# Performance work log

Measured on AMD Instinct MI355X. Metric: run time of the kernel, lower is better.

Reference implementation:

```python
import jax, jax.numpy as jnp
import numpy as np

N = 50000      # nodes
E = 800000     # edges
D = 256        # num_feat == num_hidden == out_dim
G = 64         # graphs in batch
C = 64         # num_classes
L = 2          # cells (layers)
S = 2          # GNN steps per cell
SCALE = 0.05


def setup_inputs() -> dict:
    key = jax.random.key(0)
    ks = jax.random.split(key, 10)
    x = jax.random.normal(ks[0], (N, D), jnp.float32)
    edge_index = jax.random.randint(ks[1], (2, E), 0, N, dtype=jnp.int64)
    edge_attr = jax.random.normal(ks[2], (E, 1), jnp.float32)
    batch = jnp.sort(jax.random.randint(ks[3], (N,), 0, G, dtype=jnp.int64))
    pre_w = jax.random.normal(ks[4], (L, 2, D, D), jnp.float32) * SCALE
    pre_b = jax.random.normal(ks[5], (L, 2, D), jnp.float32) * SCALE
    gcn_w = jax.random.normal(ks[6], (L, S, D, D), jnp.float32) * SCALE
    gcn_b = jax.random.normal(ks[7], (L, S, D), jnp.float32) * SCALE
    cls_w = jax.random.normal(ks[8], (D, C), jnp.float32) * SCALE
    cls_b = jax.random.normal(ks[9], (C,), jnp.float32) * SCALE
    return {"x": x, "edge_index": edge_index, "edge_attr": edge_attr,
            "batch": batch, "pre_w": pre_w, "pre_b": pre_b,
            "gcn_w": gcn_w, "gcn_b": gcn_b, "cls_w": cls_w, "cls_b": cls_b}


def reference(x, edge_index, edge_attr, batch, pre_w, pre_b, gcn_w, gcn_b, cls_w, cls_b):
    n = x.shape[0]
    # GCNConv with self-loops and symmetric normalization (torch_geometric default)
    loops = jnp.arange(n, dtype=edge_index.dtype)
    src = jnp.concatenate([edge_index[0], loops])   # [E+N]
    dst = jnp.concatenate([edge_index[1], loops])   # [E+N]
    deg = jax.ops.segment_sum(jnp.ones_like(dst, dtype=x.dtype), dst, num_segments=n)
    dinv = jax.lax.rsqrt(deg)                        # deg >= 1 due to self loops
    norm = (dinv[src] * dinv[dst])[:, None]          # [E+N, 1]

    def gcn(h, w, b):
        hw = h @ w                                   # [N, D]
        msg = hw[src] * norm                         # gather + scale
        return jax.ops.segment_sum(msg, dst, num_segments=n) + b

    def cell(s0, s1, l):
        s0 = s0 @ pre_w[l, 0] + pre_b[l, 0]
        s1 = s1 @ pre_w[l, 1] + pre_b[l, 1]
        states = [s0, s1]
        for i, idx in enumerate((0, 1)):             # NAS indices [0, 1]
            states.append(gcn(states[idx], gcn_w[l, i], gcn_b[l, i]))
        # concat='add': tmp = states[2]; then accumulate states[2:] again
        tmp = states[2]
        for st in states[2:]:
            tmp = tmp + st                           # = 2*s2 + s3 (faithful)
        return tmp

    s0 = s1 = x
    for l in range(L):
        s0, s1 = s1, cell(s0, s1, l)
    out = s1                                         # [N, D]

    g = cls_b.shape[0] if False else G
    counts = jax.ops.segment_sum(jnp.ones((n,), x.dtype), batch, num_segments=G)
    mean_pool = jax.ops.segment_sum(out, batch, num_segments=G) / jnp.maximum(counts, 1.0)[:, None]
    max_pool = jax.ops.segment_max(out, batch, num_segments=G)
    max_pool = jnp.where(counts[:, None] > 0, max_pool, 0.0)
    pooled = mean_pool + max_pool                    # [G, D]
    return pooled @ cls_w + cls_b                    # [G, C]
```

## Files before the change

### kernel.cpp

```cpp
#include <hip/hip_runtime.h>

typedef __attribute__((ext_vector_type(8))) short bf16x8;
typedef __attribute__((ext_vector_type(4))) float f32x4;

__device__ inline float bf2f(unsigned short u) {
    union { float f; unsigned int i; } v; v.i = ((unsigned int)u) << 16; return v.f;
}
__device__ inline unsigned short f2bf(float f) {
    union { float f; unsigned int u; } v; v.f = f;
    unsigned int x = v.u;
    unsigned int r = x + 0x7FFFu + ((x >> 16) & 1u);
    return (unsigned short)(r >> 16);
}
__device__ inline unsigned int fenc(float x) {
    union { float f; unsigned int u; } v; v.f = x;
    return (v.u & 0x80000000u) ? ~v.u : (v.u | 0x80000000u);
}
__device__ inline float fdec(unsigned int k) {
    union { float f; unsigned int u; } v;
    v.u = (k & 0x80000000u) ? (k & 0x7FFFFFFFu) : ~k;
    return v.f;
}
__device__ inline float ldf(const void* p, size_t i, int f32) {
    return f32 ? ((const float*)p)[i] : bf2f(((const unsigned short*)p)[i]);
}
__device__ inline int ldi(const int* p, size_t i, int i64) {
    return i64 ? p[2 * i] : p[i];
}

__global__ __launch_bounds__(256)
void k_detect(const unsigned short* __restrict__ xu, int xstride,
              const int* __restrict__ ei, int estride, int* __restrict__ flags) {
    __shared__ int cnt, orv;
    if (threadIdx.x == 0) { cnt = 0; orv = 0; }
    __syncthreads();
    int c = 0, o = 0;
    for (int s = 0; s < 4; ++s) {
        int j = threadIdx.x * 4 + s;
        size_t k = (size_t)j * xstride;
        unsigned short u = xu[2 * k];
        int e = (u >> 7) & 0xFF;
        if (e >= 100 && e <= 140) ++c;
        size_t idx = (size_t)j * estride;
        o |= ei[2 * idx + 1];
    }
    atomicAdd(&cnt, c); atomicOr(&orv, o);
    __syncthreads();
    if (threadIdx.x == 0) {
        flags[0] = (cnt < 768) ? 1 : 0;
        flags[1] = (orv == 0) ? 1 : 0;
    }
}

__global__ void k_zero(int* __restrict__ hist, int* __restrict__ cursor,
                       float* __restrict__ psum, unsigned int* __restrict__ pkey,
                       int* __restrict__ pcnt, int N) {
    int t = blockIdx.x * 256 + threadIdx.x;
    if (t < N) hist[t] = 0;
    else if (t < 2 * N) cursor[t - N] = 0;
    else if (t < 2 * N + 16384) psum[t - 2 * N] = 0.f;
    else if (t < 2 * N + 32768) pkey[t - 2 * N - 16384] = 0u;
    else if (t < 2 * N + 32768 + 64) pcnt[t - 2 * N - 32768] = 0;
}

__global__ __launch_bounds__(256)
void k_cvt(const void* __restrict__ X, unsigned short* __restrict__ Xb,
           size_t nelem, const int* __restrict__ flags) {
    int f = flags[0];
    size_t i = ((size_t)blockIdx.x * 256 + threadIdx.x) * 8;
    if (i >= nelem) return;
    if (f) {
        const float* s = (const float*)X + i;
        float4 f0 = *(const float4*)s;
        float4 f1 = *(const float4*)(s + 4);
        int4 o;
        o.x = (int)f2bf(f0.x) | ((int)f2bf(f0.y) << 16);
        o.y = (int)f2bf(f0.z) | ((int)f2bf(f0.w) << 16);
        o.z = (int)f2bf(f1.x) | ((int)f2bf(f1.y) << 16);
        o.w = (int)f2bf(f1.z) | ((int)f2bf(f1.w) << 16);
        *(int4*)(Xb + i) = o;
    } else {
        *(int4*)(Xb + i) = *(const int4*)((const unsigned short*)X + i);
    }
}

__global__ __launch_bounds__(256)
void k_cvtw(const void* __restrict__ pre_w, const void* __restrict__ gcn_w,
            unsigned short* __restrict__ Pb, unsigned short* __restrict__ Gt,
            const int* __restrict__ flags) {
    __shared__ float tile[64][65];
    const int i = blockIdx.y;
    const int m0 = (blockIdx.x & 3) * 64;
    const int n0 = (blockIdx.x >> 2) * 64;
    const int f = flags[0];
    const size_t base = (size_t)i * 65536;
#pragma unroll
    for (int q = 0; q < 16; ++q) {
        int idx = q * 256 + threadIdx.x;
        int r = idx >> 6, c = idx & 63;
        size_t src = base + (size_t)(m0 + r) * 256 + n0 + c;
        Pb[src] = f2bf(ldf(pre_w, src, f));
        tile[r][c] = ldf(gcn_w, src, f);
    }
    __syncthreads();
#pragma unroll
    for (int q = 0; q < 16; ++q) {
        int idx = q * 256 + threadIdx.x;
        int r = idx >> 6, c = idx & 63;
        Gt[base + (size_t)(n0 + r) * 256 + m0 + c] = f2bf(tile[c][r]);
    }
}

__global__ __launch_bounds__(256)
void k_prepw(const unsigned short* __restrict__ Pb, const unsigned short* __restrict__ Gt,
             unsigned short* __restrict__ Wt0, unsigned short* __restrict__ Wt1) {
    const int which = blockIdx.y;
    const int wid = threadIdx.x >> 6, lane = threadIdx.x & 63;
    const int tile = blockIdx.x * 4 + wid;
    const int n0 = (tile >> 4) * 16, k0 = (tile & 15) * 16;
    const int l15 = lane & 15, hi = lane >> 4;
    size_t base0, base1 = 0;
    if (which == 0)      { base0 = 0; base1 = 65536; }
    else if (which == 1) { base0 = 2 * 65536; }
    else                 { base0 = 3 * 65536; }
    f32x4 acc0 = {}, acc1 = {};
    const unsigned short* ga = Gt + base0 + (size_t)(n0 + l15) * 256 + hi * 8;
    const unsigned short* pa = Pb + base0 + (size_t)(k0 + l15) * 256 + hi * 8;
    const unsigned short* gb = Gt + base1 + (size_t)(n0 + l15) * 256 + hi * 8;
    const unsigned short* pb = Pb + base1 + (size_t)(k0 + l15) * 256 + hi * 8;
#pragma unroll
    for (int kt = 0; kt < 8; ++kt) {
        bf16x8 a0 = *(const bf16x8*)(ga + kt * 32);
        bf16x8 b0 = *(const bf16x8*)(pa + kt * 32);
        acc0 = __builtin_amdgcn_mfma_f32_16x16x32_bf16(a0, b0, acc0, 0, 0, 0);
        if (which == 0) {
            bf16x8 a1 = *(const bf16x8*)(gb + kt * 32);
            bf16x8 b1 = *(const bf16x8*)(pb + kt * 32);
            acc1 = __builtin_amdgcn_mfma_f32_16x16x32_bf16(a1, b1, acc1, 0, 0, 0);
        }
    }
#pragma unroll
    for (int j = 0; j < 4; ++j) {
        int n = n0 + hi * 4 + j;
        int k = k0 + l15;
        if (which == 0)      Wt0[(size_t)n * 256 + k]       = f2bf(2.f * acc0[j] + acc1[j]);
        else if (which == 1) Wt1[(size_t)n * 512 + k]       = f2bf(2.f * acc0[j]);
        else                 Wt1[(size_t)n * 512 + 256 + k] = f2bf(acc0[j]);
    }
}

__global__ __launch_bounds__(256)
void k_prepb(const void* __restrict__ pre_b, const unsigned short* __restrict__ Gt,
             const void* __restrict__ gcn_b,
             float* __restrict__ cvec, float* __restrict__ dvec,
             const int* __restrict__ flags) {
    __shared__ float pb[2][256];
    const int l = blockIdx.x, n = threadIdx.x;
    const int f = flags[0];
    pb[0][n] = ldf(pre_b, (size_t)(l * 2 + 0) * 256 + n, f);
    pb[1][n] = ldf(pre_b, (size_t)(l * 2 + 1) * 256 + n, f);
    __syncthreads();
    const unsigned short* g0 = Gt + (size_t)(l * 2 + 0) * 65536 + (size_t)n * 256;
    const unsigned short* g1 = Gt + (size_t)(l * 2 + 1) * 65536 + (size_t)n * 256;
    float a = 0.f, b = 0.f;
#pragma unroll 4
    for (int mc = 0; mc < 32; ++mc) {
        bf16x8 v0 = *(const bf16x8*)(g0 + mc * 8);
        bf16x8 v1 = *(const bf16x8*)(g1 + mc * 8);
#pragma unroll
        for (int u = 0; u < 8; ++u) {
            a += pb[0][mc * 8 + u] * bf2f((unsigned short)v0[u]);
            b += pb[1][mc * 8 + u] * bf2f((unsigned short)v1[u]);
        }
    }
    cvec[l * 256 + n] = 2.f * a + b;
    dvec[l * 256 + n] = 2.f * ldf(gcn_b, (size_t)(l * 2 + 0) * 256 + n, f)
                            + ldf(gcn_b, (size_t)(l * 2 + 1) * 256 + n, f);
}

__global__ void k_hist(const int* __restrict__ ei, int E, int N,
                       int* __restrict__ hist, const int* __restrict__ flags) {
    int e = blockIdx.x * 256 + threadIdx.x;
    if (e >= E) return;
    int i64 = flags[1];
    int d = ldi(ei, (size_t)E + e, i64); d = d < 0 ? 0 : (d >= N ? N - 1 : d);
    atomicAdd(&hist[d], 1);
}

__global__ __launch_bounds__(256)
void k_scan1(const int* __restrict__ hist, int* __restrict__ pre,
             int* __restrict__ bsum, int N) {
    __shared__ int s[256];
    int i = blockIdx.x * 256 + threadIdx.x;
    int v = (i < N) ? hist[i] : 0;
    s[threadIdx.x] = v;
    __syncthreads();
    for (int off = 1; off < 256; off <<= 1) {
        int t = (threadIdx.x >= off) ? s[threadIdx.x - off] : 0;
        __syncthreads();
        s[threadIdx.x] += t;
        __syncthreads();
    }
    if (i < N) pre[i] = s[threadIdx.x] - v;
    if (threadIdx.x == 255) bsum[blockIdx.x] = s[255];
}

__global__ __launch_bounds__(256)
void k_scan2(const int* __restrict__ bsum, int* __restrict__ boff,
             int* __restrict__ rowptr, int nb, int N) {
    __shared__ int s[256];
    int t = threadIdx.x;
    int v = (t < nb) ? bsum[t] : 0;
    s[t] = v;
    __syncthreads();
    for (int off = 1; off < 256; off <<= 1) {
        int x = (t >= off) ? s[t - off] : 0;
        __syncthreads();
        s[t] += x;
        __syncthreads();
    }
    if (t < nb) boff[t] = s[t] - v;
    if (t == nb - 1) rowptr[N] = s[t];
}

__global__ __launch_bounds__(256)
void k_scan3(const int* __restrict__ hist, const int* __restrict__ pre,
             const int* __restrict__ boff, int* __restrict__ rowptr,
             float* __restrict__ dinv, int N) {
    int i = blockIdx.x * 256 + threadIdx.x;
    if (i < N) {
        rowptr[i] = pre[i] + boff[blockIdx.x];
        dinv[i] = rsqrtf((float)(hist[i] + 1));
    }
}

__global__ void k_scatter(const int* __restrict__ ei, int E, int N,
                          const int* __restrict__ rowptr, int* __restrict__ cursor,
                          int* __restrict__ col, const int* __restrict__ flags) {
    int e = blockIdx.x * 256 + threadIdx.x;
    if (e >= E) return;
    int i64 = flags[1];
    int s = ldi(ei, (size_t)e, i64);     s = s < 0 ? 0 : (s >= N ? N - 1 : s);
    int d = ldi(ei, (size_t)E + e, i64); d = d < 0 ? 0 : (d >= N ? N - 1 : d);
    int pos = rowptr[d] + atomicAdd(&cursor[d], 1);
    col[pos] = s;
}

__global__ __launch_bounds__(512)
void k_gemm(const unsigned short* __restrict__ Xb, const unsigned short* __restrict__ Yb,
            const unsigned short* __restrict__ Wt, const float* __restrict__ cvec,
            const float* __restrict__ dinv, unsigned short* __restrict__ out,
            int M, int K) {
    __shared__ char ldsb[49152];
    const int tid = threadIdx.x;
    const int lane = tid & 63;
    const int wid = tid >> 6;
    const int wm = wid >> 2, wn = wid & 3;
    const int l15 = lane & 15, hi = lane >> 4;
    const int row0 = blockIdx.x * 128;

    const int ar = tid >> 3, acb = tid & 7;
    int agrow = row0 + ar; if (agrow > M - 1) agrow = M - 1;
    const size_t abase = (size_t)agrow * 256 + acb * 8;

    f32x4 acc[4][4] = {};
    const int KT = K / 64;
    int4 ra[2], rw[4];

    {
        const unsigned short* Asrc = Xb;
        ra[0] = *(const int4*)(Asrc + abase);
        {
            int id = 512 + tid; int r = id >> 3, cb = id & 7;
            int grow = row0 + r; if (grow > M - 1) grow = M - 1;
            ra[1] = *(const int4*)(Asrc + (size_t)grow * 256 + cb * 8);
        }
#pragma unroll
        for (int q = 0; q < 4; ++q) {
            int id = q * 512 + tid; int r = id >> 3, cb = id & 7;
            rw[q] = *(const int4*)(Wt + (size_t)r * K + cb * 8);
        }
    }

    for (int kt = 0; kt < KT; ++kt) {
        __syncthreads();
        {
            int sw = (acb * 16) ^ ((ar & 7) << 4);
            *(int4*)(ldsb + ar * 128 + sw) = ra[0];
            int id = 512 + tid; int r = id >> 3, cb = id & 7;
            int sw1 = (cb * 16) ^ ((r & 7) << 4);
            *(int4*)(ldsb + r * 128 + sw1) = ra[1];
        }
#pragma unroll
        for (int q = 0; q < 4; ++q) {
            int id = q * 512 + tid; int r = id >> 3, cb = id & 7;
            int sw = (cb * 16) ^ ((r & 7) << 4);
            *(int4*)(ldsb + 16384 + r * 128 + sw) = rw[q];
        }
        __syncthreads();
        if (kt + 1 < KT) {
            const int k1 = (kt + 1) * 64;
            const unsigned short* Asrc = (k1 < 256) ? Xb : Yb;
            const int ak1 = (k1 < 256) ? k1 : k1 - 256;
            ra[0] = *(const int4*)(Asrc + abase + ak1);
            {
                int id = 512 + tid; int r = id >> 3, cb = id & 7;
                int grow = row0 + r; if (grow > M - 1) grow = M - 1;
                ra[1] = *(const int4*)(Asrc + (size_t)grow * 256 + ak1 + cb * 8);
            }
#pragma unroll
            for (int q = 0; q < 4; ++q) {
                int id = q * 512 + tid; int r = id >> 3, cb = id & 7;
                rw[q] = *(const int4*)(Wt + (size_t)r * K + k1 + cb * 8);
            }
        }
#pragma unroll
        for (int kk = 0; kk < 2; ++kk) {
            bf16x8 af[4], bfr[4];
            int byte = kk * 64 + (hi << 4);
#pragma unroll
            for (int m = 0; m < 4; ++m) {
                int r = wm * 64 + m * 16 + l15;
                af[m] = *(const bf16x8*)(ldsb + r * 128 + (byte ^ ((r & 7) << 4)));
            }
#pragma unroll
            for (int n = 0; n < 4; ++n) {
                int r = wn * 64 + n * 16 + l15;
                bfr[n] = *(const bf16x8*)(ldsb + 16384 + r * 128 + (byte ^ ((r & 7) << 4)));
            }
#pragma unroll
            for (int m = 0; m < 4; ++m)
#pragma unroll
                for (int n = 0; n < 4; ++n)
                    acc[m][n] = __builtin_amdgcn_mfma_f32_16x16x32_bf16(af[m], bfr[n], acc[m][n], 0, 0, 0);
        }
    }
    for (int half = 0; half < 2; ++half) {
        __syncthreads();
        if (wm == half) {
#pragma unroll
            for (int m = 0; m < 4; ++m) {
#pragma unroll
                for (int j = 0; j < 4; ++j) {
                    int rl = m * 16 + hi * 4 + j;
                    int grow = row0 + half * 64 + rl;
                    if (grow < M) {
                        float di = dinv[grow];
#pragma unroll
                        for (int n = 0; n < 4; ++n) {
                            int colc = wn * 64 + n * 16 + l15;
                            float v = (acc[m][n][j] + cvec[colc]) * di;
                            *(unsigned short*)(ldsb + rl * 512 + colc * 2) = f2bf(v);
                        }
                    }
                }
            }
        }
        __syncthreads();
#pragma unroll
        for (int p = 0; p < 4; ++p) {
            int rl = p * 16 + (tid >> 5);
            int cb = tid & 31;
            int grow = row0 + half * 64 + rl;
            if (grow < M)
                *(int4*)(out + (size_t)grow * 256 + cb * 8) = *(const int4*)(ldsb + rl * 512 + cb * 16);
        }
    }
}

__global__ __launch_bounds__(256)
void k_agg(const unsigned short* __restrict__ U, const int* __restrict__ rowptr,
           const int* __restrict__ col, const float* __restrict__ dinv,
           const float* __restrict__ dvec, unsigned short* __restrict__ Y, int N) {
    int wave = (blockIdx.x * 256 + threadIdx.x) >> 6;
    int lane = threadIdx.x & 63;
    int nA = wave * 2, nB = nA + 1;
    if (nA >= N) return;
    const bool hasB = (nB < N);
    const size_t loff = (size_t)lane * 4;

    ushort4 sa = *(const ushort4*)(U + (size_t)nA * 256 + loff);
    float a0 = bf2f(sa.x), a1 = bf2f(sa.y), a2 = bf2f(sa.z), a3 = bf2f(sa.w);
    float b0 = 0.f, b1 = 0.f, b2 = 0.f, b3 = 0.f;
    int eA = rowptr[nA], endA = rowptr[nA + 1];
    int eB = 0, endB = 0;
    if (hasB) {
        ushort4 sb = *(const ushort4*)(U + (size_t)nB * 256 + loff);
        b0 = bf2f(sb.x); b1 = bf2f(sb.y); b2 = bf2f(sb.z); b3 = bf2f(sb.w);
        eB = rowptr[nB]; endB = rowptr[nB + 1];
    }

    while (eA + 8 <= endA && eB + 8 <= endB) {
        int sA[8], sB[8];
#pragma unroll
        for (int u = 0; u < 8; ++u) {
            sA[u] = __builtin_amdgcn_readfirstlane(col[eA + u]);
            sB[u] = __builtin_amdgcn_readfirstlane(col[eB + u]);
        }
        ushort4 vA[8], vB[8];
#pragma unroll
        for (int u = 0; u < 8; ++u) {
            vA[u] = *(const ushort4*)(U + (size_t)sA[u] * 256 + loff);
            vB[u] = *(const ushort4*)(U + (size_t)sB[u] * 256 + loff);
        }
#pragma unroll
        for (int u = 0; u < 8; ++u) {
            a0 += bf2f(vA[u].x); a1 += bf2f(vA[u].y);
            a2 += bf2f(vA[u].z); a3 += bf2f(vA[u].w);
            b0 += bf2f(vB[u].x); b1 += bf2f(vB[u].y);
            b2 += bf2f(vB[u].z); b3 += bf2f(vB[u].w);
        }
        eA += 8; eB += 8;
    }
    for (; eA + 8 <= endA; eA += 8) {
        int s[8]; ushort4 v[8];
#pragma unroll
        for (int u = 0; u < 8; ++u) s[u] = __builtin_amdgcn_readfirstlane(col[eA + u]);
#pragma unroll
        for (int u = 0; u < 8; ++u) v[u] = *(const ushort4*)(U + (size_t)s[u] * 256 + loff);
#pragma unroll
        for (int u = 0; u < 8; ++u) {
            a0 += bf2f(v[u].x); a1 += bf2f(v[u].y);
            a2 += bf2f(v[u].z); a3 += bf2f(v[u].w);
        }
    }
    for (; eA < endA; ++eA) {
        int s = __builtin_amdgcn_readfirstlane(col[eA]);
        ushort4 v = *(const ushort4*)(U + (size_t)s * 256 + loff);
        a0 += bf2f(v.x); a1 += bf2f(v.y); a2 += bf2f(v.z); a3 += bf2f(v.w);
    }
    if (hasB) {
        for (; eB + 8 <= endB; eB += 8) {
            int s[8]; ushort4 v[8];
#pragma unroll
            for (int u = 0; u < 8; ++u) s[u] = __builtin_amdgcn_readfirstlane(col[eB + u]);
#pragma unroll
            for (int u = 0; u < 8; ++u) v[u] = *(const ushort4*)(U + (size_t)s[u] * 256 + loff);
#pragma unroll
            for (int u = 0; u < 8; ++u) {
                b0 += bf2f(v[u].x); b1 += bf2f(v[u].y);
                b2 += bf2f(v[u].z); b3 += bf2f(v[u].w);
            }
        }
        for (; eB < endB; ++eB) {
            int s = __builtin_amdgcn_readfirstlane(col[eB]);
            ushort4 v = *(const ushort4*)(U + (size_t)s * 256 + loff);
            b0 += bf2f(v.x); b1 += bf2f(v.y); b2 += bf2f(v.z); b3 += bf2f(v.w);
        }
    }

    const int f = lane * 4;
    const float d0 = dvec[f + 0], d1 = dvec[f + 1], d2 = dvec[f + 2], d3 = dvec[f + 3];
    {
        float di = dinv[nA];
        ushort4 o;
        o.x = f2bf(a0 * di + d0); o.y = f2bf(a1 * di + d1);
        o.z = f2bf(a2 * di + d2); o.w = f2bf(a3 * di + d3);
        *(ushort4*)(Y + (size_t)nA * 256 + loff) = o;
    }
    if (hasB) {
        float di = dinv[nB];
        ushort4 o;
        o.x = f2bf(b0 * di + d0); o.y = f2bf(b1 * di + d1);
        o.z = f2bf(b2 * di + d2); o.w = f2bf(b3 * di + d3);
        *(ushort4*)(Y + (size_t)nB * 256 + loff) = o;
    }
}

__global__ __launch_bounds__(256)
void k_pool(const unsigned short* __restrict__ Y, const int* __restrict__ batch, int N,
            float* __restrict__ psum, unsigned int* __restrict__ pkey, int* __restrict__ pcnt,
            const int* __restrict__ flags) {
    int f = threadIdx.x;
    int base = blockIdx.x * 64;
    if (base >= N) return;
    int i64 = flags[1];
    int g0 = ldi(batch, base, i64); int curg = g0 < 0 ? 0 : (g0 > 63 ? 63 : g0);
    float s = 0.f, mx = -__builtin_inff(); int cnt = 0;
#pragma unroll 4
    for (int r = 0; r < 64; ++r) {
        int node = base + r;
        if (node >= N) break;
        int g = ldi(batch, node, i64); g = g < 0 ? 0 : (g > 63 ? 63 : g);
        if (g != curg) {
            atomicAdd(&psum[curg * 256 + f], s);
            atomicMax(&pkey[curg * 256 + f], fenc(mx));
            if (f == 0) atomicAdd(&pcnt[curg], cnt);
            curg = g; s = 0.f; mx = -__builtin_inff(); cnt = 0;
        }
        float v = bf2f(Y[(size_t)node * 256 + f]);
        s += v; mx = fmaxf(mx, v); ++cnt;
    }
    atomicAdd(&psum[curg * 256 + f], s);
    atomicMax(&pkey[curg * 256 + f], fenc(mx));
    if (f == 0) atomicAdd(&pcnt[curg], cnt);
}

__global__ __launch_bounds__(64)
void k_cls(const float* __restrict__ psum, const unsigned int* __restrict__ pkey,
           const int* __restrict__ pcnt, const void* __restrict__ clsw,
           const void* __restrict__ clsb, float* __restrict__ outf,
           unsigned short* __restrict__ outu, const int* __restrict__ flags) {
    __shared__ float pooled[256];
    int g = blockIdx.x, c = threadIdx.x;
    int f = flags[0];
    int cnt = pcnt[g];
    for (int m = c; m < 256; m += 64) {
        float mean = psum[g * 256 + m] / (float)(cnt > 0 ? cnt : 1);
        float mx = (cnt > 0) ? fdec(pkey[g * 256 + m]) : 0.f;
        pooled[m] = mean + mx;
    }
    __syncthreads();
    float a = ldf(clsb, c, f);
#pragma unroll 8
    for (int m = 0; m < 256; ++m) a += pooled[m] * ldf(clsw, (size_t)m * 64 + c, f);
    if (f) outf[g * 64 + c] = a;
    else   outu[g * 64 + c] = f2bf(a);
}

extern "C" void kernel_launch(void* const* d_in, const int* in_sizes, int n_in,
                              void* d_out, int out_size, void* d_ws, size_t ws_size,
                              hipStream_t stream) {
    const void*           X     = d_in[0];
    const int*            EI    = (const int*)d_in[1];
    const int*            BATCH = (const int*)d_in[3];
    const void*           PREW  = d_in[4];
    const void*           PREB  = d_in[5];
    const void*           GCNW  = d_in[6];
    const void*           GCNB  = d_in[7];
    const void*           CLSW  = d_in[8];
    const void*           CLSB  = d_in[9];

    const int N = in_sizes[3];
    const int E = in_sizes[1] / 2;
    const int NB = (N + 255) / 256;

    char* ws = (char*)d_ws;
    size_t off = 0;
    auto alloc = [&](size_t b) { size_t o = off; off += (b + 255) & ~(size_t)255; return o; };
    int*            flags  = (int*)(ws + alloc(256));
    float*          dinv   = (float*)(ws + alloc((size_t)N * 4));
    int*            hist   = (int*)(ws + alloc((size_t)N * 4));
    int*            cursor = (int*)(ws + alloc((size_t)N * 4));
    int*            rowptr = (int*)(ws + alloc((size_t)(N + 1) * 4));
    int*            pre    = (int*)(ws + alloc((size_t)N * 4));
    int*            bsum   = (int*)(ws + alloc((size_t)NB * 4));
    int*            boff   = (int*)(ws + alloc((size_t)NB * 4));
    int*            col    = (int*)(ws + alloc((size_t)E * 4));
    unsigned short* Pb     = (unsigned short*)(ws + alloc(4 * 65536 * 2));
    unsigned short* Gt     = (unsigned short*)(ws + alloc(4 * 65536 * 2));
    unsigned short* Wt0    = (unsigned short*)(ws + alloc(256 * 256 * 2));
    unsigned short* Wt1    = (unsigned short*)(ws + alloc(256 * 512 * 2));
    float*          cvec   = (float*)(ws + alloc(512 * 4));
    float*          dvec   = (float*)(ws + alloc(512 * 4));
    float*          psum   = (float*)(ws + alloc(64 * 256 * 4));
    unsigned int*   pkey   = (unsigned int*)(ws + alloc(64 * 256 * 4));
    int*            pcnt   = (int*)(ws + alloc(64 * 4));
    unsigned short* Xb     = (unsigned short*)(ws + alloc((size_t)N * 256 * 2));
    unsigned short* U      = (unsigned short*)(ws + alloc((size_t)N * 256 * 2));
    unsigned short* Y      = (unsigned short*)(ws + alloc((size_t)N * 256 * 2));

    int zt = 2 * N + 32768 + 64;
    k_zero<<<(zt + 255) / 256, 256, 0, stream>>>(hist, cursor, psum, pkey, pcnt, N);

    int xstride = (in_sizes[0] / 2) / 1024; if (xstride < 1) xstride = 1;
    int estride = E / 1024;                 if (estride < 1) estride = 1;
    k_detect<<<1, 256, 0, stream>>>((const unsigned short*)X, xstride, EI, estride, flags);

    size_t xelem = (size_t)N * 256;
    k_cvt<<<(int)((xelem / 8 + 255) / 256), 256, 0, stream>>>(X, Xb, xelem, flags);

    k_hist<<<(E + 255) / 256, 256, 0, stream>>>(EI, E, N, hist, flags);
    k_scan1<<<NB, 256, 0, stream>>>(hist, pre, bsum, N);
    k_scan2<<<1, 256, 0, stream>>>(bsum, boff, rowptr, NB, N);
    k_scan3<<<NB, 256, 0, stream>>>(hist, pre, boff, rowptr, dinv, N);
    k_scatter<<<(E + 255) / 256, 256, 0, stream>>>(EI, E, N, rowptr, cursor, col, flags);

    k_cvtw<<<dim3(16, 4), 256, 0, stream>>>(PREW, GCNW, Pb, Gt, flags);
    k_prepw<<<dim3(64, 3), 256, 0, stream>>>(Pb, Gt, Wt0, Wt1);
    k_prepb<<<2, 256, 0, stream>>>(PREB, Gt, GCNB, cvec, dvec, flags);

    int ggrid = (N + 127) / 128;
    int agrid = (N + 7) / 8;
    k_gemm<<<ggrid, 512, 0, stream>>>(Xb, U, Wt0, cvec, dinv, U, N, 256);
    k_agg<<<agrid, 256, 0, stream>>>(U, rowptr, col, dinv, dvec, Y, N);
    k_gemm<<<ggrid, 512, 0, stream>>>(Xb, Y, Wt1, cvec + 256, dinv, U, N, 512);
    k_agg<<<agrid, 256, 0, stream>>>(U, rowptr, col, dinv, dvec + 256, Y, N);
    k_pool<<<(N + 63) / 64, 256, 0, stream>>>(Y, BATCH, N, psum, pkey, pcnt, flags);
    k_cls<<<64, 64, 0, stream>>>(psum, pkey, pcnt, CLSW, CLSB,
                                 (float*)d_out, (unsigned short*)d_out, flags);
}
```

Before: 406.3 us.

## Load GEMM MFMA fragments directly from global and fuse detect with zero init

The GEMM main loop no longer stages A and W tiles through shared memory with barriers. Each wave now loads its MFMA operand fragments straight from global memory into registers, with a two-deep register double buffer over K steps of 32. This removes the LDS writes, the LDS reads and the per-tile syncs, at the cost of redundant global/L2 reads: four waves share each A row block and two share each W column block. Separately, the detect and zero kernels are merged into one launch to save a kernel dispatch.

Result: no change. 413.9 us (+1.9%).

```diff
diff --git a/kernel.cpp b/kernel.cpp
--- a/kernel.cpp
+++ b/kernel.cpp
@@ -28,34 +28,34 @@
     return i64 ? p[2 * i] : p[i];
 }
 
-__global__ __launch_bounds__(256)
-void k_detect(const unsigned short* __restrict__ xu, int xstride,
-              const int* __restrict__ ei, int estride, int* __restrict__ flags) {
-    __shared__ int cnt, orv;
-    if (threadIdx.x == 0) { cnt = 0; orv = 0; }
-    __syncthreads();
-    int c = 0, o = 0;
-    for (int s = 0; s < 4; ++s) {
-        int j = threadIdx.x * 4 + s;
-        size_t k = (size_t)j * xstride;
-        unsigned short u = xu[2 * k];
-        int e = (u >> 7) & 0xFF;
-        if (e >= 100 && e <= 140) ++c;
-        size_t idx = (size_t)j * estride;
-        o |= ei[2 * idx + 1];
-    }
-    atomicAdd(&cnt, c); atomicOr(&orv, o);
-    __syncthreads();
-    if (threadIdx.x == 0) {
-        flags[0] = (cnt < 768) ? 1 : 0;
-        flags[1] = (orv == 0) ? 1 : 0;
-    }
-}
-
-__global__ void k_zero(int* __restrict__ hist, int* __restrict__ cursor,
+__global__ void k_init(const unsigned short* __restrict__ xu, int xstride,
+                       const int* __restrict__ ei, int estride, int* __restrict__ flags,
+                       int* __restrict__ hist, int* __restrict__ cursor,
                        float* __restrict__ psum, unsigned int* __restrict__ pkey,
                        int* __restrict__ pcnt, int N) {
-    int t = blockIdx.x * 256 + threadIdx.x;
+    if (blockIdx.x == 0) {
+        __shared__ int cnt, orv;
+        if (threadIdx.x == 0) { cnt = 0; orv = 0; }
+        __syncthreads();
+        int c = 0, o = 0;
+        for (int s = 0; s < 4; ++s) {
+            int j = threadIdx.x * 4 + s;
+            size_t k = (size_t)j * xstride;
+            unsigned short u = xu[2 * k];
+            int e = (u >> 7) & 0xFF;
+            if (e >= 100 && e <= 140) ++c;
+            size_t idx = (size_t)j * estride;
+            o |= ei[2 * idx + 1];
+        }
+        atomicAdd(&cnt, c); atomicOr(&orv, o);
+        __syncthreads();
+        if (threadIdx.x == 0) {
+            flags[0] = (cnt < 768) ? 1 : 0;
+            flags[1] = (orv == 0) ? 1 : 0;
+        }
+        return;
+    }
+    int t = (blockIdx.x - 1) * 256 + threadIdx.x;
     if (t < N) hist[t] = 0;
     else if (t < 2 * N) cursor[t - N] = 0;
     else if (t < 2 * N + 16384) psum[t - 2 * N] = 0.f;
@@ -251,7 +251,7 @@
             const unsigned short* __restrict__ Wt, const float* __restrict__ cvec,
             const float* __restrict__ dinv, unsigned short* __restrict__ out,
             int M, int K) {
-    __shared__ char ldsb[49152];
+    __shared__ char ldsb[32768];
     const int tid = threadIdx.x;
     const int lane = tid & 63;
     const int wid = tid >> 6;
@@ -259,82 +259,47 @@
     const int l15 = lane & 15, hi = lane >> 4;
     const int row0 = blockIdx.x * 128;
 
-    const int ar = tid >> 3, acb = tid & 7;
-    int agrow = row0 + ar; if (agrow > M - 1) agrow = M - 1;
-    const size_t abase = (size_t)agrow * 256 + acb * 8;
+    unsigned int aoff[4], woff[4];
+#pragma unroll
+    for (int m = 0; m < 4; ++m) {
+        int r = row0 + wm * 64 + m * 16 + l15;
+        if (r > M - 1) r = M - 1;
+        aoff[m] = (unsigned int)r * 256u + hi * 8;
+    }
+#pragma unroll
+    for (int n = 0; n < 4; ++n)
+        woff[n] = (unsigned int)(wn * 64 + n * 16 + l15) * (unsigned int)K + hi * 8;
 
     f32x4 acc[4][4] = {};
-    const int KT = K / 64;
-    int4 ra[2], rw[4];
-
-    {
-        const unsigned short* Asrc = Xb;
-        ra[0] = *(const int4*)(Asrc + abase);
-        {
-            int id = 512 + tid; int r = id >> 3, cb = id & 7;
-            int grow = row0 + r; if (grow > M - 1) grow = M - 1;
-            ra[1] = *(const int4*)(Asrc + (size_t)grow * 256 + cb * 8);
-        }
-#pragma unroll
-        for (int q = 0; q < 4; ++q) {
-            int id = q * 512 + tid; int r = id >> 3, cb = id & 7;
-            rw[q] = *(const int4*)(Wt + (size_t)r * K + cb * 8);
-        }
-    }
-
-    for (int kt = 0; kt < KT; ++kt) {
-        __syncthreads();
-        {
-            int sw = (acb * 16) ^ ((ar & 7) << 4);
-            *(int4*)(ldsb + ar * 128 + sw) = ra[0];
-            int id = 512 + tid; int r = id >> 3, cb = id & 7;
-            int sw1 = (cb * 16) ^ ((r & 7) << 4);
-            *(int4*)(ldsb + r * 128 + sw1) = ra[1];
-        }
-#pragma unroll
-        for (int q = 0; q < 4; ++q) {
-            int id = q * 512 + tid; int r = id >> 3, cb = id & 7;
-            int sw = (cb * 16) ^ ((r & 7) << 4);
-            *(int4*)(ldsb + 16384 + r * 128 + sw) = rw[q];
-        }
-        __syncthreads();
-        if (kt + 1 < KT) {
-            const int k1 = (kt + 1) * 64;
-            const unsigned short* Asrc = (k1 < 256) ? Xb : Yb;
-            const int ak1 = (k1 < 256) ? k1 : k1 - 256;
-            ra[0] = *(const int4*)(Asrc + abase + ak1);
-            {
-                int id = 512 + tid; int r = id >> 3, cb = id & 7;
-                int grow = row0 + r; if (grow > M - 1) grow = M - 1;
-                ra[1] = *(const int4*)(Asrc + (size_t)grow * 256 + ak1 + cb * 8);
-            }
-#pragma unroll
-            for (int q = 0; q < 4; ++q) {
-                int id = q * 512 + tid; int r = id >> 3, cb = id & 7;
-                rw[q] = *(const int4*)(Wt + (size_t)r * K + k1 + cb * 8);
-            }
-        }
-#pragma unroll
-        for (int kk = 0; kk < 2; ++kk) {
-            bf16x8 af[4], bfr[4];
-            int byte = kk * 64 + (hi << 4);
-#pragma unroll
-            for (int m = 0; m < 4; ++m) {
-                int r = wm * 64 + m * 16 + l15;
-                af[m] = *(const bf16x8*)(ldsb + r * 128 + (byte ^ ((r & 7) << 4)));
-            }
-#pragma unroll
-            for (int n = 0; n < 4; ++n) {
-                int r = wn * 64 + n * 16 + l15;
-                bfr[n] = *(const bf16x8*)(ldsb + 16384 + r * 128 + (byte ^ ((r & 7) << 4)));
-            }
-#pragma unroll
-            for (int m = 0; m < 4; ++m)
-#pragma unroll
-                for (int n = 0; n < 4; ++n)
-                    acc[m][n] = __builtin_amdgcn_mfma_f32_16x16x32_bf16(af[m], bfr[n], acc[m][n], 0, 0, 0);
-        }
-    }
+    const int S = K / 32;
+
+    bf16x8 fa0[4], fb0[4], fa1[4], fb1[4];
+    auto LOAD = [&](int s, bf16x8 (&fA)[4], bf16x8 (&fB)[4]) {
+        const unsigned short* Asrc = (s < 8) ? Xb : Yb;
+        const unsigned int ak = (unsigned int)(s & 7) * 32u;
+#pragma unroll
+        for (int m = 0; m < 4; ++m)
+            fA[m] = *(const bf16x8*)(Asrc + aoff[m] + ak);
+#pragma unroll
+        for (int n = 0; n < 4; ++n)
+            fB[n] = *(const bf16x8*)(Wt + woff[n] + (unsigned int)s * 32u);
+    };
+    auto DOMFMA = [&](bf16x8 (&fA)[4], bf16x8 (&fB)[4]) {
+#pragma unroll
+        for (int m = 0; m < 4; ++m)
+#pragma unroll
+            for (int n = 0; n < 4; ++n)
+                acc[m][n] = __builtin_amdgcn_mfma_f32_16x16x32_bf16(fA[m], fB[n], acc[m][n], 0, 0, 0);
+    };
+
+    LOAD(0, fa0, fb0);
+    for (int s = 0; s < S; s += 2) {
+        LOAD(s + 1, fa1, fb1);
+        DOMFMA(fa0, fb0);
+        if (s + 2 < S) LOAD(s + 2, fa0, fb0);
+        DOMFMA(fa1, fb1);
+    }
+
     for (int half = 0; half < 2; ++half) {
         __syncthreads();
         if (wm == half) {
@@ -560,12 +525,12 @@
     unsigned short* U      = (unsigned short*)(ws + alloc((size_t)N * 256 * 2));
     unsigned short* Y      = (unsigned short*)(ws + alloc((size_t)N * 256 * 2));
 
-    int zt = 2 * N + 32768 + 64;
-    k_zero<<<(zt + 255) / 256, 256, 0, stream>>>(hist, cursor, psum, pkey, pcnt, N);
-
     int xstride = (in_sizes[0] / 2) / 1024; if (xstride < 1) xstride = 1;
     int estride = E / 1024;                 if (estride < 1) estride = 1;
-    k_detect<<<1, 256, 0, stream>>>((const unsigned short*)X, xstride, EI, estride, flags);
+    int zt = 2 * N + 32768 + 64;
+    k_init<<<1 + (zt + 255) / 256, 256, 0, stream>>>((const unsigned short*)X, xstride,
+                                                     EI, estride, flags,
+                                                     hist, cursor, psum, pkey, pcnt, N);
 
     size_t xelem = (size_t)N * 256;
     k_cvt<<<(int)((xelem / 8 + 255) / 256), 256, 0, stream>>>(X, Xb, xelem, flags);
```

## Fuse input fp32-to-bf16 conversion into first GEMM and merge init kernels

Applied to the files above, without the earlier changes.

Removes the standalone conversion kernel by having the first GEMM read raw X (fp32 or bf16), convert it in registers, stage it into LDS and also write the bf16 copy to Xb for the later GEMM. The detect and zero kernels are merged into a single init launch. This saves one full pass over X and two launches. In exchange the first GEMM issues wider fp32 loads and extra global writes inside its main loop, and Xb is padded by 128 rows to absorb clamped writes.

Result: no change. 404.7 us (-0.4%).

```diff
diff --git a/kernel.cpp b/kernel.cpp
--- a/kernel.cpp
+++ b/kernel.cpp
@@ -27,61 +27,48 @@
 __device__ inline int ldi(const int* p, size_t i, int i64) {
     return i64 ? p[2 * i] : p[i];
 }
-
-__global__ __launch_bounds__(256)
-void k_detect(const unsigned short* __restrict__ xu, int xstride,
-              const int* __restrict__ ei, int estride, int* __restrict__ flags) {
-    __shared__ int cnt, orv;
-    if (threadIdx.x == 0) { cnt = 0; orv = 0; }
-    __syncthreads();
-    int c = 0, o = 0;
-    for (int s = 0; s < 4; ++s) {
-        int j = threadIdx.x * 4 + s;
-        size_t k = (size_t)j * xstride;
-        unsigned short u = xu[2 * k];
-        int e = (u >> 7) & 0xFF;
-        if (e >= 100 && e <= 140) ++c;
-        size_t idx = (size_t)j * estride;
-        o |= ei[2 * idx + 1];
-    }
-    atomicAdd(&cnt, c); atomicOr(&orv, o);
-    __syncthreads();
-    if (threadIdx.x == 0) {
-        flags[0] = (cnt < 768) ? 1 : 0;
-        flags[1] = (orv == 0) ? 1 : 0;
-    }
-}
-
-__global__ void k_zero(int* __restrict__ hist, int* __restrict__ cursor,
+__device__ inline int4 cvt8(float4 a, float4 b) {
+    int4 o;
+    o.x = (int)f2bf(a.x) | ((int)f2bf(a.y) << 16);
+    o.y = (int)f2bf(a.z) | ((int)f2bf(a.w) << 16);
+    o.z = (int)f2bf(b.x) | ((int)f2bf(b.y) << 16);
+    o.w = (int)f2bf(b.z) | ((int)f2bf(b.w) << 16);
+    return o;
+}
+
+__global__ void k_init(const unsigned short* __restrict__ xu, int xstride,
+                       const int* __restrict__ ei, int estride, int* __restrict__ flags,
+                       int* __restrict__ hist, int* __restrict__ cursor,
                        float* __restrict__ psum, unsigned int* __restrict__ pkey,
                        int* __restrict__ pcnt, int N) {
-    int t = blockIdx.x * 256 + threadIdx.x;
+    if (blockIdx.x == 0) {
+        __shared__ int cnt, orv;
+        if (threadIdx.x == 0) { cnt = 0; orv = 0; }
+        __syncthreads();
+        int c = 0, o = 0;
+        for (int s = 0; s < 4; ++s) {
+            int j = threadIdx.x * 4 + s;
+            size_t k = (size_t)j * xstride;
+            unsigned short u = xu[2 * k];
+            int e = (u >> 7) & 0xFF;
+            if (e >= 100 && e <= 140) ++c;
+            size_t idx = (size_t)j * estride;
+            o |= ei[2 * idx + 1];
+        }
+        atomicAdd(&cnt, c); atomicOr(&orv, o);
+        __syncthreads();
+        if (threadIdx.x == 0) {
+            flags[0] = (cnt < 768) ? 1 : 0;
+            flags[1] = (orv == 0) ? 1 : 0;
+        }
+        return;
+    }
+    int t = (blockIdx.x - 1) * 256 + threadIdx.x;
     if (t < N) hist[t] = 0;
     else if (t < 2 * N) cursor[t - N] = 0;
     else if (t < 2 * N + 16384) psum[t - 2 * N] = 0.f;
     else if (t < 2 * N + 32768) pkey[t - 2 * N - 16384] = 0u;
     else if (t < 2 * N + 32768 + 64) pcnt[t - 2 * N - 32768] = 0;
-}
-
-__global__ __launch_bounds__(256)
-void k_cvt(const void* __restrict__ X, unsigned short* __restrict__ Xb,
-           size_t nelem, const int* __restrict__ flags) {
-    int f = flags[0];
-    size_t i = ((size_t)blockIdx.x * 256 + threadIdx.x) * 8;
-    if (i >= nelem) return;
-    if (f) {
-        const float* s = (const float*)X + i;
-        float4 f0 = *(const float4*)s;
-        float4 f1 = *(const float4*)(s + 4);
-        int4 o;
-        o.x = (int)f2bf(f0.x) | ((int)f2bf(f0.y) << 16);
-        o.y = (int)f2bf(f0.z) | ((int)f2bf(f0.w) << 16);
-        o.z = (int)f2bf(f1.x) | ((int)f2bf(f1.y) << 16);
-        o.w = (int)f2bf(f1.z) | ((int)f2bf(f1.w) << 16);
-        *(int4*)(Xb + i) = o;
-    } else {
-        *(int4*)(Xb + i) = *(const int4*)((const unsigned short*)X + i);
-    }
 }
 
 __global__ __launch_bounds__(256)
@@ -244,6 +231,127 @@
     int d = ldi(ei, (size_t)E + e, i64); d = d < 0 ? 0 : (d >= N ? N - 1 : d);
     int pos = rowptr[d] + atomicAdd(&cursor[d], 1);
     col[pos] = s;
+}
+
+__global__ __launch_bounds__(512)
+void k_gemm1(const void* __restrict__ Xraw, unsigned short* __restrict__ Xb,
+             const unsigned short* __restrict__ Wt, const float* __restrict__ cvec,
+             const float* __restrict__ dinv, unsigned short* __restrict__ out,
+             int M, const int* __restrict__ flags) {
+    __shared__ char ldsb[49152];
+    const int tid = threadIdx.x;
+    const int lane = tid & 63;
+    const int wid = tid >> 6;
+    const int wm = wid >> 2, wn = wid & 3;
+    const int l15 = lane & 15, hi = lane >> 4;
+    const int row0 = blockIdx.x * 128;
+    const int xf32 = flags[0];
+    const int K = 256;
+
+    const int r0 = tid >> 3, cb0 = tid & 7;
+    const int r1 = (512 + tid) >> 3, cb1 = tid & 7;
+    int g0 = row0 + r0; if (g0 > M - 1) g0 = M - 1;
+    int g1 = row0 + r1; if (g1 > M - 1) g1 = M - 1;
+    const size_t ab0 = (size_t)g0 * 256 + cb0 * 8;
+    const size_t ab1 = (size_t)g1 * 256 + cb1 * 8;
+
+    f32x4 acc[4][4] = {};
+    int4 ra0, ra1, rw[4];
+    float4 rf0a, rf0b, rf1a, rf1b;
+
+    auto LOADA = [&](int ak) {
+        if (xf32) {
+            const float* s0 = (const float*)Xraw + ab0 + ak;
+            rf0a = *(const float4*)s0; rf0b = *(const float4*)(s0 + 4);
+            const float* s1 = (const float*)Xraw + ab1 + ak;
+            rf1a = *(const float4*)s1; rf1b = *(const float4*)(s1 + 4);
+        } else {
+            ra0 = *(const int4*)((const unsigned short*)Xraw + ab0 + ak);
+            ra1 = *(const int4*)((const unsigned short*)Xraw + ab1 + ak);
+        }
+    };
+    auto LOADW = [&](int k0) {
+#pragma unroll
+        for (int q = 0; q < 4; ++q) {
+            int id = q * 512 + tid; int r = id >> 3, cb = id & 7;
+            rw[q] = *(const int4*)(Wt + (size_t)r * K + k0 + cb * 8);
+        }
+    };
+
+    LOADA(0); LOADW(0);
+    for (int kt = 0; kt < 4; ++kt) {
+        const int k0 = kt * 64;
+        __syncthreads();
+        {
+            int4 v0 = xf32 ? cvt8(rf0a, rf0b) : ra0;
+            int4 v1 = xf32 ? cvt8(rf1a, rf1b) : ra1;
+            int sw0 = (cb0 * 16) ^ ((r0 & 7) << 4);
+            int sw1 = (cb1 * 16) ^ ((r1 & 7) << 4);
+            *(int4*)(ldsb + r0 * 128 + sw0) = v0;
+            *(int4*)(ldsb + r1 * 128 + sw1) = v1;
+            *(int4*)(Xb + ab0 + k0) = v0;
+            *(int4*)(Xb + ab1 + k0) = v1;
+        }
+#pragma unroll
+        for (int q = 0; q < 4; ++q) {
+            int id = q * 512 + tid; int r = id >> 3, cb = id & 7;
+            int sw = (cb * 16) ^ ((r & 7) << 4);
+            *(int4*)(ldsb + 16384 + r * 128 + sw) = rw[q];
+        }
+        __syncthreads();
+        if (kt + 1 < 4) { LOADA((kt + 1) * 64); LOADW((kt + 1) * 64); }
+#pragma unroll
+        for (int kk = 0; kk < 2; ++kk) {
+            bf16x8 af[4], bfr[4];
+            int byte = kk * 64 + (hi << 4);
+#pragma unroll
+            for (int m = 0; m < 4; ++m) {
+                int r = wm * 64 + m * 16 + l15;
+                af[m] = *(const bf16x8*)(ldsb + r * 128 + (byte ^ ((r & 7) << 4)));
+            }
+#pragma unroll
+            for (int n = 0; n < 4; ++n) {
+                int r = wn * 64 + n * 16 + l15;
+                bfr[n] = *(const bf16x8*)(ldsb + 16384 + r * 128 + (byte ^ ((r & 7) << 4)));
+            }
+#pragma unroll
+            for (int m = 0; m < 4; ++m)
+#pragma unroll
+                for (int n = 0; n < 4; ++n)
+                    acc[m][n] = __builtin_amdgcn_mfma_f32_16x16x32_bf16(af[m], bfr[n], acc[m][n], 0, 0, 0);
+        }
+    }
+    for (int half = 0; half < 2; ++half) {
+        __syncthreads();
+        if (wm == half) {
+#pragma unroll
+            for (int m = 0; m < 4; ++m) {
+#pragma unroll
+                for (int j = 0; j < 4; ++j) {
+                    int rl = m * 16 + hi * 4 + j;
+                    int grow = row0 + half * 64 + rl;
+                    if (grow < M) {
+                        float di = dinv[grow];
+#pragma unroll
+                        for (int n = 0; n < 4; ++n) {
+                            int colc = wn * 64 + n * 16 + l15;
+                            float v = (acc[m][n][j] + cvec[colc]) * di;
+                            *(unsigned short*)(ldsb + rl * 512 + colc * 2) = f2bf(v);
+                        }
+                    }
+                }
+            }
+        }
+        __syncthreads();
+#pragma unroll
+        for (int p = 0; p < 4; ++p) {
+            int rl = p * 16 + (tid >> 5);
+            int cb = tid & 31;
+            int grow = row0 + half * 64 + rl;
+            if (grow < M)
+                *(int4*)(out + (size_t)grow * 256 + cb * 8) = *(const int4*)(ldsb + rl * 512 + cb * 16);
+        }
+    }
 }
 
 __global__ __launch_bounds__(512)
@@ -556,19 +664,16 @@
     float*          psum   = (float*)(ws + alloc(64 * 256 * 4));
     unsigned int*   pkey   = (unsigned int*)(ws + alloc(64 * 256 * 4));
     int*            pcnt   = (int*)(ws + alloc(64 * 4));
-    unsigned short* Xb     = (unsigned short*)(ws + alloc((size_t)N * 256 * 2));
+    unsigned short* Xb     = (unsigned short*)(ws + alloc((size_t)(N + 128) * 256 * 2));
     unsigned short* U      = (unsigned short*)(ws + alloc((size_t)N * 256 * 2));
     unsigned short* Y      = (unsigned short*)(ws + alloc((size_t)N * 256 * 2));
 
-    int zt = 2 * N + 32768 + 64;
-    k_zero<<<(zt + 255) / 256, 256, 0, stream>>>(hist, cursor, psum, pkey, pcnt, N);
-
     int xstride = (in_sizes[0] / 2) / 1024; if (xstride < 1) xstride = 1;
     int estride = E / 1024;                 if (estride < 1) estride = 1;
-    k_detect<<<1, 256, 0, stream>>>((const unsigned short*)X, xstride, EI, estride, flags);
-
-    size_t xelem = (size_t)N * 256;
-    k_cvt<<<(int)((xelem / 8 + 255) / 256), 256, 0, stream>>>(X, Xb, xelem, flags);
+    int zt = 2 * N + 32768 + 64;
+    k_init<<<1 + (zt + 255) / 256, 256, 0, stream>>>((const unsigned short*)X, xstride,
+                                                     EI, estride, flags,
+                                                     hist, cursor, psum, pkey, pcnt, N);
 
     k_hist<<<(E + 255) / 256, 256, 0, stream>>>(EI, E, N, hist, flags);
     k_scan1<<<NB, 256, 0, stream>>>(hist, pre, bsum, N);
@@ -582,7 +687,7 @@
 
     int ggrid = (N + 127) / 128;
     int agrid = (N + 7) / 8;
-    k_gemm<<<ggrid, 512, 0, stream>>>(Xb, U, Wt0, cvec, dinv, U, N, 256);
+    k_gemm1<<<ggrid, 512, 0, stream>>>(X, Xb, Wt0, cvec, dinv, U, N, flags);
     k_agg<<<agrid, 256, 0, stream>>>(U, rowptr, col, dinv, dvec, Y, N);
     k_gemm<<<ggrid, 512, 0, stream>>>(Xb, Y, Wt1, cvec + 256, dinv, U, N, 512);
     k_agg<<<agrid, 256, 0, stream>>>(U, rowptr, col, dinv, dvec + 256, Y, N);
```

## Add persistent first-layer GEMM with LDS-resident weights and merge init kernels

Applied to the files above, without the earlier changes.

Adds a persistent GEMM kernel for the first K=256 projection. Each of 256 blocks loads the full 256x256 bf16 weight into 128KB of swizzled LDS once, then loops over row tiles and reads A fragments directly from global memory with double buffering, staging the epilogue through LDS for coalesced stores. This removes the per-tile reload of weights and the LDS staging of A. The flag-detection and zeroing kernels are also merged into one launch to save a kernel launch. The large LDS footprint limits occupancy to one block per CU, and the direct global A loads are strided per lane.

New measurement: 405.0 us. Within noise of the previous version (-0.3%).

```diff
diff --git a/kernel.cpp b/kernel.cpp
--- a/kernel.cpp
+++ b/kernel.cpp
@@ -28,34 +28,34 @@
     return i64 ? p[2 * i] : p[i];
 }
 
-__global__ __launch_bounds__(256)
-void k_detect(const unsigned short* __restrict__ xu, int xstride,
-              const int* __restrict__ ei, int estride, int* __restrict__ flags) {
-    __shared__ int cnt, orv;
-    if (threadIdx.x == 0) { cnt = 0; orv = 0; }
-    __syncthreads();
-    int c = 0, o = 0;
-    for (int s = 0; s < 4; ++s) {
-        int j = threadIdx.x * 4 + s;
-        size_t k = (size_t)j * xstride;
-        unsigned short u = xu[2 * k];
-        int e = (u >> 7) & 0xFF;
-        if (e >= 100 && e <= 140) ++c;
-        size_t idx = (size_t)j * estride;
-        o |= ei[2 * idx + 1];
-    }
-    atomicAdd(&cnt, c); atomicOr(&orv, o);
-    __syncthreads();
-    if (threadIdx.x == 0) {
-        flags[0] = (cnt < 768) ? 1 : 0;
-        flags[1] = (orv == 0) ? 1 : 0;
-    }
-}
-
-__global__ void k_zero(int* __restrict__ hist, int* __restrict__ cursor,
+__global__ void k_init(const unsigned short* __restrict__ xu, int xstride,
+                       const int* __restrict__ ei, int estride, int* __restrict__ flags,
+                       int* __restrict__ hist, int* __restrict__ cursor,
                        float* __restrict__ psum, unsigned int* __restrict__ pkey,
                        int* __restrict__ pcnt, int N) {
-    int t = blockIdx.x * 256 + threadIdx.x;
+    if (blockIdx.x == 0) {
+        __shared__ int cnt, orv;
+        if (threadIdx.x == 0) { cnt = 0; orv = 0; }
+        __syncthreads();
+        int c = 0, o = 0;
+        for (int s = 0; s < 4; ++s) {
+            int j = threadIdx.x * 4 + s;
+            size_t k = (size_t)j * xstride;
+            unsigned short u = xu[2 * k];
+            int e = (u >> 7) & 0xFF;
+            if (e >= 100 && e <= 140) ++c;
+            size_t idx = (size_t)j * estride;
+            o |= ei[2 * idx + 1];
+        }
+        atomicAdd(&cnt, c); atomicOr(&orv, o);
+        __syncthreads();
+        if (threadIdx.x == 0) {
+            flags[0] = (cnt < 768) ? 1 : 0;
+            flags[1] = (orv == 0) ? 1 : 0;
+        }
+        return;
+    }
+    int t = (blockIdx.x - 1) * 256 + threadIdx.x;
     if (t < N) hist[t] = 0;
     else if (t < 2 * N) cursor[t - N] = 0;
     else if (t < 2 * N + 16384) psum[t - 2 * N] = 0.f;
@@ -244,6 +244,102 @@
     int d = ldi(ei, (size_t)E + e, i64); d = d < 0 ? 0 : (d >= N ? N - 1 : d);
     int pos = rowptr[d] + atomicAdd(&cursor[d], 1);
     col[pos] = s;
+}
+
+__global__ __launch_bounds__(512)
+void k_gemm1p(const unsigned short* __restrict__ Xb, const unsigned short* __restrict__ Wt,
+              const float* __restrict__ cvec, const float* __restrict__ dinv,
+              unsigned short* __restrict__ out, int M, int ntiles) {
+    __shared__ char ldsb[147456];
+    const int tid = threadIdx.x;
+    const int lane = tid & 63;
+    const int wid = tid >> 6;
+    const int wm = wid >> 2, wn = wid & 3;
+    const int l15 = lane & 15, hi = lane >> 4;
+
+#pragma unroll
+    for (int q = 0; q < 16; ++q) {
+        int id = q * 512 + tid;
+        int r = id >> 5, cb = id & 31;
+        int4 v = *(const int4*)(Wt + (size_t)r * 256 + cb * 8);
+        int sw = (cb * 16) ^ ((r & 7) << 4);
+        *(int4*)(ldsb + r * 512 + sw) = v;
+    }
+    __syncthreads();
+
+    for (int tile = blockIdx.x; tile < ntiles; tile += gridDim.x) {
+        const int row0 = tile * 128;
+        unsigned int aoff[4];
+#pragma unroll
+        for (int m = 0; m < 4; ++m) {
+            int r = row0 + wm * 64 + m * 16 + l15;
+            if (r > M - 1) r = M - 1;
+            aoff[m] = (unsigned int)r * 256u + hi * 8;
+        }
+        f32x4 acc[4][4] = {};
+        bf16x8 fa0[4], fa1[4];
+        auto LOADA = [&](int s, bf16x8 (&fA)[4]) {
+            unsigned int ak = (unsigned int)s * 32u;
+#pragma unroll
+            for (int m = 0; m < 4; ++m)
+                fA[m] = *(const bf16x8*)(Xb + aoff[m] + ak);
+        };
+        auto STEP = [&](int s, bf16x8 (&fA)[4]) {
+            bf16x8 fb[4];
+            int byte = s * 64 + hi * 16;
+#pragma unroll
+            for (int n = 0; n < 4; ++n) {
+                int r = wn * 64 + n * 16 + l15;
+                fb[n] = *(const bf16x8*)(ldsb + r * 512 + (byte ^ ((r & 7) << 4)));
+            }
+#pragma unroll
+            for (int m = 0; m < 4; ++m)
+#pragma unroll
+                for (int n = 0; n < 4; ++n)
+                    acc[m][n] = __builtin_amdgcn_mfma_f32_16x16x32_bf16(fA[m], fb[n], acc[m][n], 0, 0, 0);
+        };
+        LOADA(0, fa0);
+#pragma unroll
+        for (int s = 0; s < 8; s += 2) {
+            LOADA(s + 1, fa1);
+            STEP(s, fa0);
+            if (s + 2 < 8) LOADA(s + 2, fa0);
+            STEP(s + 1, fa1);
+        }
+        char* eb = ldsb + 131072;
+        for (int h = 0; h < 4; ++h) {
+            __syncthreads();
+            if (wm == (h >> 1)) {
+#pragma unroll
+                for (int mm = 0; mm < 2; ++mm) {
+                    int m = (h & 1) * 2 + mm;
+#pragma unroll
+                    for (int j = 0; j < 4; ++j) {
+                        int rl = mm * 16 + hi * 4 + j;
+                        int grow = row0 + h * 32 + rl;
+                        if (grow < M) {
+                            float di = dinv[grow];
+#pragma unroll
+                            for (int n = 0; n < 4; ++n) {
+                                int colc = wn * 64 + n * 16 + l15;
+                                float v = (acc[m][n][j] + cvec[colc]) * di;
+                                *(unsigned short*)(eb + rl * 512 + colc * 2) = f2bf(v);
+                            }
+                        }
+                    }
+                }
+            }
+            __syncthreads();
+#pragma unroll
+            for (int q = 0; q < 2; ++q) {
+                int id = q * 512 + tid;
+                int rl = id >> 5, cb = id & 31;
+                int grow = row0 + h * 32 + rl;
+                if (grow < M)
+                    *(int4*)(out + (size_t)grow * 256 + cb * 8) = *(const int4*)(eb + rl * 512 + cb * 16);
+            }
+        }
+    }
 }
 
 __global__ __launch_bounds__(512)
@@ -556,16 +652,16 @@
     float*          psum   = (float*)(ws + alloc(64 * 256 * 4));
     unsigned int*   pkey   = (unsigned int*)(ws + alloc(64 * 256 * 4));
     int*            pcnt   = (int*)(ws + alloc(64 * 4));
-    unsigned short* Xb     = (unsigned short*)(ws + alloc((size_t)N * 256 * 2));
+    unsigned short* Xb     = (unsigned short*)(ws + alloc((size_t)(N + 128) * 256 * 2));
     unsigned short* U      = (unsigned short*)(ws + alloc((size_t)N * 256 * 2));
     unsigned short* Y      = (unsigned short*)(ws + alloc((size_t)N * 256 * 2));
 
-    int zt = 2 * N + 32768 + 64;
-    k_zero<<<(zt + 255) / 256, 256, 0, stream>>>(hist, cursor, psum, pkey, pcnt, N);
-
     int xstride = (in_sizes[0] / 2) / 1024; if (xstride < 1) xstride = 1;
     int estride = E / 1024;                 if (estride < 1) estride = 1;
-    k_detect<<<1, 256, 0, stream>>>((const unsigned short*)X, xstride, EI, estride, flags);
+    int zt = 2 * N + 32768 + 64;
+    k_init<<<1 + (zt + 255) / 256, 256, 0, stream>>>((const unsigned short*)X, xstride,
+                                                     EI, estride, flags,
+                                                     hist, cursor, psum, pkey, pcnt, N);
 
     size_t xelem = (size_t)N * 256;
     k_cvt<<<(int)((xelem / 8 + 255) / 256), 256, 0, stream>>>(X, Xb, xelem, flags);
@@ -580,11 +676,11 @@
     k_prepw<<<dim3(64, 3), 256, 0, stream>>>(Pb, Gt, Wt0, Wt1);
     k_prepb<<<2, 256, 0, stream>>>(PREB, Gt, GCNB, cvec, dvec, flags);
 
-    int ggrid = (N + 127) / 128;
+    int ntiles = (N + 127) / 128;
     int agrid = (N + 7) / 8;
-    k_gemm<<<ggrid, 512, 0, stream>>>(Xb, U, Wt0, cvec, dinv, U, N, 256);
+    k_gemm1p<<<256, 512, 0, stream>>>(Xb, Wt0, cvec, dinv, U, N, ntiles);
     k_agg<<<agrid, 256, 0, stream>>>(U, rowptr, col, dinv, dvec, Y, N);
-    k_gemm<<<ggrid, 512, 0, stream>>>(Xb, Y, Wt1, cvec + 256, dinv, U, N, 512);
+    k_gemm<<<ntiles, 512, 0, stream>>>(Xb, Y, Wt1, cvec + 256, dinv, U, N, 512);
     k_agg<<<agrid, 256, 0, stream>>>(U, rowptr, col, dinv, dvec + 256, Y, N);
     k_pool<<<(N + 63) / 64, 256, 0, stream>>>(Y, BATCH, N, psum, pkey, pcnt, flags);
     k_cls<<<64, 64, 0, stream>>>(psum, pkey, pcnt, CLSW, CLSB,
```
